# Kernel tuning notes

Measured on AMD Instinct MI355X. Metric: run time of the kernel, lower is better.

Reference implementation:

```python
import jax, jax.numpy as jnp
import numpy as np

E, H, I = 5, 768, 1024  # num_experts, hidden_dim, intermediate_dim
TOP_K = 2


def setup_inputs() -> dict:
    key = jax.random.key(0)
    ks = jax.random.split(key, 6)
    s = 0.02
    return {
        "x": jax.random.normal(ks[0], (4, 2048, H), dtype=jnp.float32),
        "router_w": jax.random.normal(ks[1], (E, H), dtype=jnp.float32) * s,  # torch Linear (out,in)
        "router_b": jnp.zeros((E,), dtype=jnp.float32),
        "gate_w": jax.random.normal(ks[2], (E, H, I), dtype=jnp.float32) * s,
        "up_w": jax.random.normal(ks[3], (E, H, I), dtype=jnp.float32) * s,
        "down_w": jax.random.normal(ks[4], (E, I, H), dtype=jnp.float32) * s,
    }


def reference(x, router_w, router_b, gate_w, up_w, down_w):
    B, S, Hd = x.shape
    xf = x.reshape(-1, Hd)                       # [T, H]
    T = xf.shape[0]
    # Router: linear (with bias) -> softmax -> top-2 -> renormalize
    logits = xf @ router_w.T + router_b          # [T, E]
    scores = jax.nn.softmax(logits, axis=-1)
    vals, idx = jax.lax.top_k(scores, TOP_K)     # [T, 2]
    vals = vals / jnp.sum(vals, axis=-1, keepdims=True)
    # Dense combine weights: zero for unselected experts (same math as the
    # per-expert gather/scatter loop in the original module).
    comb = jnp.zeros((T, gate_w.shape[0]), dtype=x.dtype)
    comb = comb.at[jnp.arange(T)[:, None], idx].add(vals)  # [T, E]
    # SwiGLU per expert, vectorized over experts
    g = jnp.einsum('th,ehi->tei', xf, gate_w)    # [T, E, I]
    u = jnp.einsum('th,ehi->tei', xf, up_w)
    y = jnp.einsum('tei,eih->teh', jax.nn.silu(g) * u, down_w)  # [T, E, H]
    out = jnp.einsum('teh,te->th', y, comb)
    return out.reshape(B, S, Hd)
```

## Files before the change

### kernel.cpp

```cpp
#include <hip/hip_runtime.h>
#include <hip/hip_bf16.h>
#include <cstdint>
#include <cstddef>

#define T_TOK 8192
#define H_DIM 768
#define I_DIM 1024
#define N_EXP 5
#define MAXTILE 136

typedef short v8s __attribute__((ext_vector_type(8)));
typedef float v4f __attribute__((ext_vector_type(4)));

static __device__ __forceinline__ unsigned short f2bf(float f) {
    union { float f; unsigned int u; } v; v.f = f;
    unsigned int u = v.u;
    unsigned int r = (u + 0x7fffu + ((u >> 16) & 1u)) >> 16;
    return (unsigned short)r;
}
static __device__ __forceinline__ float bf2f(unsigned short s) {
    union { unsigned int u; float f; } v; v.u = ((unsigned int)s) << 16; return v.f;
}

static __device__ __forceinline__ void async16(const unsigned short* g, unsigned short* l) {
    __builtin_amdgcn_global_load_lds(
        (const __attribute__((address_space(1))) unsigned int*)g,
        (__attribute__((address_space(3))) unsigned int*)l, 16, 0, 0);
}

__global__ void k_transp_wi(const float* __restrict__ gw, const float* __restrict__ uw,
                            unsigned short* __restrict__ wbt) {
    __shared__ float tile[32][33];
    int z = blockIdx.z;
    int e = z % N_EXP;
    int isUp = z >= N_EXP;
    const float* src = (isUp ? uw : gw) + (size_t)e * H_DIM * I_DIM;
    int c0 = blockIdx.x * 32, r0 = blockIdx.y * 32;
    int tx = threadIdx.x, ty = threadIdx.y;
#pragma unroll
    for (int i = 0; i < 4; i++)
        tile[ty * 4 + i][tx] = src[(size_t)(r0 + ty * 4 + i) * I_DIM + c0 + tx];
    __syncthreads();
#pragma unroll
    for (int i = 0; i < 4; i++) {
        int c = c0 + ty * 4 + i;
        int row = (c >> 4) * 32 + (c & 15) + (isUp ? 16 : 0);
        wbt[((size_t)e * 2 * I_DIM + row) * H_DIM + r0 + tx] = f2bf(tile[tx][ty * 4 + i]);
    }
}

__global__ void k_transp_d(const float* __restrict__ dw, unsigned short* __restrict__ dbt) {
    __shared__ float tile[32][33];
    int e = blockIdx.z;
    const float* src = dw + (size_t)e * I_DIM * H_DIM;
    unsigned short* dst = dbt + (size_t)e * I_DIM * H_DIM;
    int c0 = blockIdx.x * 32, r0 = blockIdx.y * 32;
    int tx = threadIdx.x, ty = threadIdx.y;
#pragma unroll
    for (int i = 0; i < 4; i++)
        tile[ty * 4 + i][tx] = src[(size_t)(r0 + ty * 4 + i) * H_DIM + c0 + tx];
    __syncthreads();
#pragma unroll
    for (int i = 0; i < 4; i++)
        dst[(size_t)(c0 + ty * 4 + i) * I_DIM + r0 + tx] = f2bf(tile[tx][ty * 4 + i]);
}

__global__ void k_router_a(const float* __restrict__ x, const float* __restrict__ rw,
                           const float* __restrict__ rb,
                           unsigned short* __restrict__ xb,
                           int* __restrict__ top2e, float2* __restrict__ top2w) {
    const int wave = threadIdx.x >> 6, lane = threadIdx.x & 63;
    const int t = blockIdx.x * 4 + wave;
    const float* xr = x + (size_t)t * H_DIM;
    unsigned short* xbr = xb + (size_t)t * H_DIM;
    float acc[N_EXP];
#pragma unroll
    for (int e = 0; e < N_EXP; e++) acc[e] = 0.f;
#pragma unroll
    for (int j = 0; j < H_DIM / 256; j++) {
        int idx = j * 256 + lane * 4;
        float4 xv = *(const float4*)(xr + idx);
        ushort4 o;
        o.x = f2bf(xv.x); o.y = f2bf(xv.y); o.z = f2bf(xv.z); o.w = f2bf(xv.w);
        *(ushort4*)(xbr + idx) = o;
#pragma unroll
        for (int e = 0; e < N_EXP; e++) {
            float4 wv = *(const float4*)(rw + e * H_DIM + idx);
            acc[e] += xv.x * wv.x + xv.y * wv.y + xv.z * wv.z + xv.w * wv.w;
        }
    }
#pragma unroll
    for (int s = 32; s > 0; s >>= 1) {
#pragma unroll
        for (int e = 0; e < N_EXP; e++) acc[e] += __shfl_down(acc[e], s);
    }
    if (lane == 0) {
        float l[N_EXP];
#pragma unroll
        for (int e = 0; e < N_EXP; e++) l[e] = acc[e] + rb[e];
        int i1 = 0;
#pragma unroll
        for (int e = 1; e < N_EXP; e++) if (l[e] > l[i1]) i1 = e;
        int i2 = (i1 == 0) ? 1 : 0;
#pragma unroll
        for (int e = 0; e < N_EXP; e++) if (e != i1 && l[e] > l[i2]) i2 = e;
        float w1 = 1.f / (1.f + __expf(l[i2] - l[i1]));
        top2e[t] = i1 | (i2 << 8);
        top2w[t] = make_float2(w1, 1.f - w1);
    }
}

__global__ void k_router_b(const int* __restrict__ top2e, const float2* __restrict__ top2w,
                           int* __restrict__ cnt, int* __restrict__ tokslot,
                           float* __restrict__ pweight) {
    __shared__ int lcnt[N_EXP], lbase[N_EXP];
    const int tid = threadIdx.x;
    if (tid < N_EXP) lcnt[tid] = 0;
    __syncthreads();
    const int t = blockIdx.x * 256 + tid;
    const int pe = top2e[t];
    const float2 wv = top2w[t];
    const int e1 = pe & 0xff, e2 = pe >> 8;
    const int s1 = atomicAdd(&lcnt[e1], 1);
    const int s2 = atomicAdd(&lcnt[e2], 1);
    __syncthreads();
    if (tid < N_EXP) lbase[tid] = atomicAdd(&cnt[tid], lcnt[tid]);
    __syncthreads();
    const int p1 = lbase[e1] + s1;
    tokslot[e1 * T_TOK + p1] = t; pweight[e1 * T_TOK + p1] = wv.x;
    const int p2 = lbase[e2] + s2;
    tokslot[e2 * T_TOK + p2] = t | (1 << 16); pweight[e2 * T_TOK + p2] = wv.y;
}

__global__ void k_tiles(const int* __restrict__ cnt, int4* __restrict__ tiles) {
    const int tid = threadIdx.x;
    if (tid < MAXTILE) tiles[tid] = make_int4(-1, 0, 0, 0);
    __syncthreads();
    if (tid == 0) {
        int off = 0, idx = 0;
        for (int e = 0; e < N_EXP; e++) {
            int cn = cnt[e];
            for (int m0 = 0; m0 < cn; m0 += 128)
                tiles[idx++] = make_int4(e, m0, off, cn);
            off += cn;
        }
    }
}

__launch_bounds__(256, 2)
__global__ void k_gateup(const unsigned short* __restrict__ xb,
                         const unsigned short* __restrict__ wbt,
                         const int4* __restrict__ tiles,
                         const int* __restrict__ tokslot,
                         const float* __restrict__ pweight,
                         unsigned short* __restrict__ hbuf) {
    const int4 td = tiles[blockIdx.x];
    const int e = td.x;
    if (e < 0) return;
    const int m0 = td.y, offe = td.z, cn = td.w;
    const int n0 = blockIdx.y * 64;

    __shared__ __align__(16) unsigned short ldsA[128 * 32];
    __shared__ __align__(16) unsigned short ldsB[128 * 32];
    __shared__ int tokLds[128];
    __shared__ float pwLds[128];

    const int tid = threadIdx.x;
    if (tid < 128) {
        int gr = m0 + tid;
        int tk = 0; float pw = 0.f;
        if (gr < cn) { tk = tokslot[e * T_TOK + gr] & 0xFFFF; pw = pweight[e * T_TOK + gr]; }
        tokLds[tid] = tk; pwLds[tid] = pw;
    }
    __syncthreads();

    const int lane = tid & 63;
    const int wave = tid >> 6;
    const int fm = lane & 15, quad = lane >> 4;

    const int srow = wave * 16 + (lane >> 2);
    const int scol = (lane & 3) * 8;
    const unsigned short* aG1 = xb + (size_t)tokLds[srow] * H_DIM + scol;
    const unsigned short* aG2 = xb + (size_t)tokLds[64 + srow] * H_DIM + scol;
    const unsigned short* bG1 = wbt + ((size_t)e * 2 * I_DIM + n0 * 2 + srow) * H_DIM + scol;
    const unsigned short* bG2 = wbt + ((size_t)e * 2 * I_DIM + n0 * 2 + 64 + srow) * H_DIM + scol;
    unsigned short* lA1 = ldsA + wave * 512;
    unsigned short* lA2 = ldsA + 2048 + wave * 512;
    unsigned short* lB1 = ldsB + wave * 512;
    unsigned short* lB2 = ldsB + 2048 + wave * 512;

    const int wm = (wave & 1) * 64, wnw = wave >> 1;

    v4f acc[4][4];
#pragma unroll
    for (int i = 0; i < 4; i++)
#pragma unroll
        for (int j = 0; j < 4; j++) acc[i][j] = (v4f)0.f;

    for (int kb = 0; kb < H_DIM / 32; kb++) {
        const int k0 = kb * 32;
        async16(aG1 + k0, lA1);
        async16(aG2 + k0, lA2);
        async16(bG1 + k0, lB1);
        async16(bG2 + k0, lB2);
        __syncthreads();
        v8s aF[4], bF[4];
#pragma unroll
        for (int im = 0; im < 4; im++)
            aF[im] = *(const v8s*)&ldsA[(wm + im * 16 + fm) * 32 + quad * 8];
#pragma unroll
        for (int in = 0; in < 4; in++)
            bF[in] = *(const v8s*)&ldsB[(wnw * 64 + in * 16 + fm) * 32 + quad * 8];
#pragma unroll
        for (int im = 0; im < 4; im++)
#pragma unroll
            for (int in = 0; in < 4; in++)
                acc[im][in] = __builtin_amdgcn_mfma_f32_16x16x32_bf16(aF[im], bF[in], acc[im][in], 0, 0, 0);
        __syncthreads();
    }

#pragma unroll
    for (int im = 0; im < 4; im++) {
#pragma unroll
        for (int reg = 0; reg < 4; reg++) {
            int lr = wm + im * 16 + quad * 4 + reg;
            int gr = m0 + lr;
            if (gr < cn) {
                float pw = pwLds[lr];
                size_t base = (size_t)(offe + gr) * I_DIM + n0 + wnw * 32 + fm;
#pragma unroll
                for (int j = 0; j < 2; j++) {
                    float g = acc[im][2 * j][reg];
                    float u = acc[im][2 * j + 1][reg];
                    float s = g / (1.f + __expf(-g));
                    hbuf[base + j * 16] = f2bf(s * u * pw);
                }
            }
        }
    }
}

__launch_bounds__(256, 2)
__global__ void k_down(const unsigned short* __restrict__ hbuf,
                       const unsigned short* __restrict__ dbt,
                       const int4* __restrict__ tiles,
                       const int* __restrict__ tokslot,
                       unsigned short* __restrict__ ybuf) {
    const int4 td = tiles[blockIdx.x];
    const int e = td.x;
    if (e < 0) return;
    const int m0 = td.y, offe = td.z, cn = td.w;
    const int n0 = blockIdx.y * 128;

    __shared__ __align__(16) unsigned short ldsA[128 * 32];
    __shared__ __align__(16) unsigned short ldsB[128 * 32];
    __shared__ int tokLds[128];

    const int tid = threadIdx.x;
    if (tid < 128) {
        int gr = m0 + tid;
        tokLds[tid] = (gr < cn) ? tokslot[e * T_TOK + gr] : 0;
    }
    __syncthreads();

    const int lane = tid & 63;
    const int wave = tid >> 6;
    const int fm = lane & 15, quad = lane >> 4;

    const int srow = wave * 16 + (lane >> 2);
    const int scol = (lane & 3) * 8;
    int ar1 = m0 + srow;      if (ar1 >= cn) ar1 = cn - 1;
    int ar2 = m0 + 64 + srow; if (ar2 >= cn) ar2 = cn - 1;
    const unsigned short* aG1 = hbuf + (size_t)(offe + ar1) * I_DIM + scol;
    const unsigned short* aG2 = hbuf + (size_t)(offe + ar2) * I_DIM + scol;
    const unsigned short* bG1 = dbt + ((size_t)e * H_DIM + n0 + srow) * I_DIM + scol;
    const unsigned short* bG2 = dbt + ((size_t)e * H_DIM + n0 + 64 + srow) * I_DIM + scol;
    unsigned short* lA1 = ldsA + wave * 512;
    unsigned short* lA2 = ldsA + 2048 + wave * 512;
    unsigned short* lB1 = ldsB + wave * 512;
    unsigned short* lB2 = ldsB + 2048 + wave * 512;

    const int wm = (wave & 1) * 64, wn = (wave >> 1) * 64;

    v4f acc[4][4];
#pragma unroll
    for (int i = 0; i < 4; i++)
#pragma unroll
        for (int j = 0; j < 4; j++) acc[i][j] = (v4f)0.f;

    for (int kb = 0; kb < I_DIM / 32; kb++) {
        const int k0 = kb * 32;
        async16(aG1 + k0, lA1);
        async16(aG2 + k0, lA2);
        async16(bG1 + k0, lB1);
        async16(bG2 + k0, lB2);
        __syncthreads();
        v8s aF[4], bF[4];
#pragma unroll
        for (int im = 0; im < 4; im++)
            aF[im] = *(const v8s*)&ldsA[(wm + im * 16 + fm) * 32 + quad * 8];
#pragma unroll
        for (int in = 0; in < 4; in++)
            bF[in] = *(const v8s*)&ldsB[(wn + in * 16 + fm) * 32 + quad * 8];
#pragma unroll
        for (int im = 0; im < 4; im++)
#pragma unroll
            for (int in = 0; in < 4; in++)
                acc[im][in] = __builtin_amdgcn_mfma_f32_16x16x32_bf16(aF[im], bF[in], acc[im][in], 0, 0, 0);
        __syncthreads();
    }

#pragma unroll
    for (int im = 0; im < 4; im++) {
#pragma unroll
        for (int reg = 0; reg < 4; reg++) {
            int lr = wm + im * 16 + quad * 4 + reg;
            int gr = m0 + lr;
            if (gr < cn) {
                int v = tokLds[lr];
                int tok = v & 0xFFFF, s = (v >> 16) & 1;
#pragma unroll
                for (int in = 0; in < 4; in++) {
                    int col = n0 + wn + in * 16 + fm;
                    ybuf[((size_t)s * T_TOK + tok) * H_DIM + col] = f2bf(acc[im][in][reg]);
                }
            }
        }
    }
}

__global__ void k_combine(const unsigned short* __restrict__ ybuf, float* __restrict__ out) {
    const size_t i8 = ((size_t)blockIdx.x * 256 + threadIdx.x) * 8;
    const unsigned short* y0 = ybuf + i8;
    const unsigned short* y1 = ybuf + (size_t)T_TOK * H_DIM + i8;
    ushort4 a0 = *(const ushort4*)y0, a1 = *(const ushort4*)(y0 + 4);
    ushort4 b0 = *(const ushort4*)y1, b1 = *(const ushort4*)(y1 + 4);
    float4 o0, o1;
    o0.x = bf2f(a0.x) + bf2f(b0.x); o0.y = bf2f(a0.y) + bf2f(b0.y);
    o0.z = bf2f(a0.z) + bf2f(b0.z); o0.w = bf2f(a0.w) + bf2f(b0.w);
    o1.x = bf2f(a1.x) + bf2f(b1.x); o1.y = bf2f(a1.y) + bf2f(b1.y);
    o1.z = bf2f(a1.z) + bf2f(b1.z); o1.w = bf2f(a1.w) + bf2f(b1.w);
    *(float4*)(out + i8) = o0;
    *(float4*)(out + i8 + 4) = o1;
}

extern "C" void kernel_launch(void* const* d_in, const int* in_sizes, int n_in,
                              void* d_out, int out_size, void* d_ws, size_t ws_size,
                              hipStream_t stream) {
    const float* x  = (const float*)d_in[0];
    const float* rw = (const float*)d_in[1];
    const float* rb = (const float*)d_in[2];
    const float* gw = (const float*)d_in[3];
    const float* uw = (const float*)d_in[4];
    const float* dw = (const float*)d_in[5];
    float* out = (float*)d_out;

    char* ws = (char*)d_ws;
    size_t o = 0;
    auto alloc = [&](size_t bytes) { void* p = ws + o; o += (bytes + 255) & ~255ull; return p; };
    int*   cnt     = (int*)  alloc(N_EXP * 4);
    int*   tokslot = (int*)  alloc((size_t)N_EXP * T_TOK * 4);
    float* pweight = (float*)alloc((size_t)N_EXP * T_TOK * 4);
    int*   top2e   = (int*)  alloc((size_t)T_TOK * 4);
    float2* top2w  = (float2*)alloc((size_t)T_TOK * 8);
    int4*  tiles   = (int4*) alloc((size_t)MAXTILE * 16);
    unsigned short* xb   = (unsigned short*)alloc((size_t)T_TOK * H_DIM * 2);
    unsigned short* wbt  = (unsigned short*)alloc((size_t)N_EXP * 2 * I_DIM * H_DIM * 2);
    unsigned short* dbt  = (unsigned short*)alloc((size_t)N_EXP * H_DIM * I_DIM * 2);
    unsigned short* hbuf = (unsigned short*)alloc((size_t)2 * T_TOK * I_DIM * 2);
    unsigned short* ybuf = (unsigned short*)alloc((size_t)2 * T_TOK * H_DIM * 2);

    hipMemsetAsync(cnt, 0, N_EXP * 4, stream);

    dim3 tg1(I_DIM / 32, H_DIM / 32, 2 * N_EXP);
    k_transp_wi<<<tg1, dim3(32, 8), 0, stream>>>(gw, uw, wbt);
    dim3 tg2(H_DIM / 32, I_DIM / 32, N_EXP);
    k_transp_d<<<tg2, dim3(32, 8), 0, stream>>>(dw, dbt);

    k_router_a<<<T_TOK / 4, 256, 0, stream>>>(x, rw, rb, xb, top2e, top2w);
    k_router_b<<<T_TOK / 256, 256, 0, stream>>>(top2e, top2w, cnt, tokslot, pweight);
    k_tiles<<<1, 256, 0, stream>>>(cnt, tiles);

    dim3 g1(MAXTILE, I_DIM / 64);
    k_gateup<<<g1, 256, 0, stream>>>(xb, wbt, tiles, tokslot, pweight, hbuf);

    dim3 g2(MAXTILE, H_DIM / 128);
    k_down<<<g2, 256, 0, stream>>>(hbuf, dbt, tiles, tokslot, ybuf);

    k_combine<<<(T_TOK * H_DIM) / (256 * 8), 256, 0, stream>>>(ybuf, out);
}
```

Measured before the change: 265.9 us.

## Pre-gather routed tokens into contiguous bf16 buffer and scatter-combine via inverse map

Adds a gather kernel that converts routed token rows of x to bf16 in expert-sorted contiguous order, so the gate/up GEMM loads A rows contiguously instead of through per-row token indirection. The down GEMM writes its output in sorted order, and the combine kernel uses an inverse index to sum each token's two expert rows. It also merges the two weight-transpose kernels into one launch and raises launch bounds to 4 blocks per CU. The trade is an extra gather pass and padding rows in exchange for fewer indirect loads. Padded rows past the tile end now read uninitialized workspace instead of clamped rows, but their results are discarded.

Result: slower. 299.5 us (+12.6%).

```diff
diff --git a/kernel.cpp b/kernel.cpp
--- a/kernel.cpp
+++ b/kernel.cpp
@@ -8,6 +8,7 @@
 #define I_DIM 1024
 #define N_EXP 5
 #define MAXTILE 136
+#define DROWS (2 * T_TOK)
 
 typedef short v8s __attribute__((ext_vector_type(8)));
 typedef float v4f __attribute__((ext_vector_type(4)));
@@ -28,51 +29,50 @@
         (__attribute__((address_space(3))) unsigned int*)l, 16, 0, 0);
 }
 
-__global__ void k_transp_wi(const float* __restrict__ gw, const float* __restrict__ uw,
-                            unsigned short* __restrict__ wbt) {
+__global__ void k_transp_all(const float* __restrict__ gw, const float* __restrict__ uw,
+                             const float* __restrict__ dw,
+                             unsigned short* __restrict__ wbt, unsigned short* __restrict__ dbt) {
     __shared__ float tile[32][33];
-    int z = blockIdx.z;
-    int e = z % N_EXP;
-    int isUp = z >= N_EXP;
-    const float* src = (isUp ? uw : gw) + (size_t)e * H_DIM * I_DIM;
-    int c0 = blockIdx.x * 32, r0 = blockIdx.y * 32;
-    int tx = threadIdx.x, ty = threadIdx.y;
-#pragma unroll
-    for (int i = 0; i < 4; i++)
-        tile[ty * 4 + i][tx] = src[(size_t)(r0 + ty * 4 + i) * I_DIM + c0 + tx];
-    __syncthreads();
-#pragma unroll
-    for (int i = 0; i < 4; i++) {
-        int c = c0 + ty * 4 + i;
-        int row = (c >> 4) * 32 + (c & 15) + (isUp ? 16 : 0);
-        wbt[((size_t)e * 2 * I_DIM + row) * H_DIM + r0 + tx] = f2bf(tile[tx][ty * 4 + i]);
-    }
-}
-
-__global__ void k_transp_d(const float* __restrict__ dw, unsigned short* __restrict__ dbt) {
-    __shared__ float tile[32][33];
-    int e = blockIdx.z;
-    const float* src = dw + (size_t)e * I_DIM * H_DIM;
-    unsigned short* dst = dbt + (size_t)e * I_DIM * H_DIM;
-    int c0 = blockIdx.x * 32, r0 = blockIdx.y * 32;
-    int tx = threadIdx.x, ty = threadIdx.y;
-#pragma unroll
-    for (int i = 0; i < 4; i++)
-        tile[ty * 4 + i][tx] = src[(size_t)(r0 + ty * 4 + i) * H_DIM + c0 + tx];
-    __syncthreads();
-#pragma unroll
-    for (int i = 0; i < 4; i++)
-        dst[(size_t)(c0 + ty * 4 + i) * I_DIM + r0 + tx] = f2bf(tile[tx][ty * 4 + i]);
+    const int z = blockIdx.z;
+    const int tx = threadIdx.x, ty = threadIdx.y;
+    if (z < 2 * N_EXP) {
+        if (blockIdx.y >= H_DIM / 32) return;
+        const int e = z % N_EXP;
+        const int isUp = z >= N_EXP;
+        const float* src = (isUp ? uw : gw) + (size_t)e * H_DIM * I_DIM;
+        const int c0 = blockIdx.x * 32, r0 = blockIdx.y * 32;
+#pragma unroll
+        for (int i = 0; i < 4; i++)
+            tile[ty * 4 + i][tx] = src[(size_t)(r0 + ty * 4 + i) * I_DIM + c0 + tx];
+        __syncthreads();
+#pragma unroll
+        for (int i = 0; i < 4; i++) {
+            int c = c0 + ty * 4 + i;
+            int row = (c >> 4) * 32 + (c & 15) + (isUp ? 16 : 0);
+            wbt[((size_t)e * 2 * I_DIM + row) * H_DIM + r0 + tx] = f2bf(tile[tx][ty * 4 + i]);
+        }
+    } else {
+        if (blockIdx.x >= H_DIM / 32) return;
+        const int e = z - 2 * N_EXP;
+        const float* src = dw + (size_t)e * I_DIM * H_DIM;
+        unsigned short* dst = dbt + (size_t)e * I_DIM * H_DIM;
+        const int c0 = blockIdx.x * 32, r0 = blockIdx.y * 32;
+#pragma unroll
+        for (int i = 0; i < 4; i++)
+            tile[ty * 4 + i][tx] = src[(size_t)(r0 + ty * 4 + i) * H_DIM + c0 + tx];
+        __syncthreads();
+#pragma unroll
+        for (int i = 0; i < 4; i++)
+            dst[(size_t)(c0 + ty * 4 + i) * I_DIM + r0 + tx] = f2bf(tile[tx][ty * 4 + i]);
+    }
 }
 
 __global__ void k_router_a(const float* __restrict__ x, const float* __restrict__ rw,
                            const float* __restrict__ rb,
-                           unsigned short* __restrict__ xb,
                            int* __restrict__ top2e, float2* __restrict__ top2w) {
     const int wave = threadIdx.x >> 6, lane = threadIdx.x & 63;
     const int t = blockIdx.x * 4 + wave;
     const float* xr = x + (size_t)t * H_DIM;
-    unsigned short* xbr = xb + (size_t)t * H_DIM;
     float acc[N_EXP];
 #pragma unroll
     for (int e = 0; e < N_EXP; e++) acc[e] = 0.f;
@@ -80,9 +80,6 @@
     for (int j = 0; j < H_DIM / 256; j++) {
         int idx = j * 256 + lane * 4;
         float4 xv = *(const float4*)(xr + idx);
-        ushort4 o;
-        o.x = f2bf(xv.x); o.y = f2bf(xv.y); o.z = f2bf(xv.z); o.w = f2bf(xv.w);
-        *(ushort4*)(xbr + idx) = o;
 #pragma unroll
         for (int e = 0; e < N_EXP; e++) {
             float4 wv = *(const float4*)(rw + e * H_DIM + idx);
@@ -147,12 +144,39 @@
     }
 }
 
-__launch_bounds__(256, 2)
-__global__ void k_gateup(const unsigned short* __restrict__ xb,
+__global__ void k_gather(const float* __restrict__ x, const int4* __restrict__ tiles,
+                         const int* __restrict__ tokslot, const float* __restrict__ pweight,
+                         unsigned short* __restrict__ xg, float* __restrict__ pwg,
+                         int* __restrict__ inv) {
+    const int4 td = tiles[blockIdx.x];
+    const int e = td.x;
+    if (e < 0) return;
+    const int m0 = td.y, offe = td.z, cn = td.w;
+    const int tid = threadIdx.x;
+    for (int c = tid; c < 128 * 96; c += 256) {
+        int row = c / 96, col = (c % 96) * 8;
+        int gr = m0 + row;
+        if (gr >= cn) continue;
+        int v = tokslot[e * T_TOK + gr];
+        int tok = v & 0xFFFF;
+        const float* src = x + (size_t)tok * H_DIM + col;
+        float4 a = *(const float4*)src, b = *(const float4*)(src + 4);
+        ushort4 o0; o0.x = f2bf(a.x); o0.y = f2bf(a.y); o0.z = f2bf(a.z); o0.w = f2bf(a.w);
+        ushort4 o1; o1.x = f2bf(b.x); o1.y = f2bf(b.y); o1.z = f2bf(b.z); o1.w = f2bf(b.w);
+        unsigned short* dst = xg + (size_t)(offe + gr) * H_DIM + col;
+        *(ushort4*)dst = o0; *(ushort4*)(dst + 4) = o1;
+        if ((c % 96) == 0) {
+            pwg[offe + gr] = pweight[e * T_TOK + gr];
+            inv[tok * 2 + ((v >> 16) & 1)] = offe + gr;
+        }
+    }
+}
+
+__launch_bounds__(256, 4)
+__global__ void k_gateup(const unsigned short* __restrict__ xg,
                          const unsigned short* __restrict__ wbt,
                          const int4* __restrict__ tiles,
-                         const int* __restrict__ tokslot,
-                         const float* __restrict__ pweight,
+                         const float* __restrict__ pwg,
                          unsigned short* __restrict__ hbuf) {
     const int4 td = tiles[blockIdx.x];
     const int e = td.x;
@@ -162,16 +186,10 @@
 
     __shared__ __align__(16) unsigned short ldsA[128 * 32];
     __shared__ __align__(16) unsigned short ldsB[128 * 32];
-    __shared__ int tokLds[128];
     __shared__ float pwLds[128];
 
     const int tid = threadIdx.x;
-    if (tid < 128) {
-        int gr = m0 + tid;
-        int tk = 0; float pw = 0.f;
-        if (gr < cn) { tk = tokslot[e * T_TOK + gr] & 0xFFFF; pw = pweight[e * T_TOK + gr]; }
-        tokLds[tid] = tk; pwLds[tid] = pw;
-    }
+    if (tid < 128) pwLds[tid] = pwg[offe + m0 + tid];
     __syncthreads();
 
     const int lane = tid & 63;
@@ -180,10 +198,10 @@
 
     const int srow = wave * 16 + (lane >> 2);
     const int scol = (lane & 3) * 8;
-    const unsigned short* aG1 = xb + (size_t)tokLds[srow] * H_DIM + scol;
-    const unsigned short* aG2 = xb + (size_t)tokLds[64 + srow] * H_DIM + scol;
+    const unsigned short* aG1 = xg + (size_t)(offe + m0 + srow) * H_DIM + scol;
+    const unsigned short* aG2 = aG1 + (size_t)64 * H_DIM;
     const unsigned short* bG1 = wbt + ((size_t)e * 2 * I_DIM + n0 * 2 + srow) * H_DIM + scol;
-    const unsigned short* bG2 = wbt + ((size_t)e * 2 * I_DIM + n0 * 2 + 64 + srow) * H_DIM + scol;
+    const unsigned short* bG2 = bG1 + (size_t)64 * H_DIM;
     unsigned short* lA1 = ldsA + wave * 512;
     unsigned short* lA2 = ldsA + 2048 + wave * 512;
     unsigned short* lB1 = ldsB + wave * 512;
@@ -240,12 +258,11 @@
     }
 }
 
-__launch_bounds__(256, 2)
+__launch_bounds__(256, 4)
 __global__ void k_down(const unsigned short* __restrict__ hbuf,
                        const unsigned short* __restrict__ dbt,
                        const int4* __restrict__ tiles,
-                       const int* __restrict__ tokslot,
-                       unsigned short* __restrict__ ybuf) {
+                       unsigned short* __restrict__ yd) {
     const int4 td = tiles[blockIdx.x];
     const int e = td.x;
     if (e < 0) return;
@@ -254,27 +271,18 @@
 
     __shared__ __align__(16) unsigned short ldsA[128 * 32];
     __shared__ __align__(16) unsigned short ldsB[128 * 32];
-    __shared__ int tokLds[128];
 
     const int tid = threadIdx.x;
-    if (tid < 128) {
-        int gr = m0 + tid;
-        tokLds[tid] = (gr < cn) ? tokslot[e * T_TOK + gr] : 0;
-    }
-    __syncthreads();
-
     const int lane = tid & 63;
     const int wave = tid >> 6;
     const int fm = lane & 15, quad = lane >> 4;
 
     const int srow = wave * 16 + (lane >> 2);
     const int scol = (lane & 3) * 8;
-    int ar1 = m0 + srow;      if (ar1 >= cn) ar1 = cn - 1;
-    int ar2 = m0 + 64 + srow; if (ar2 >= cn) ar2 = cn - 1;
-    const unsigned short* aG1 = hbuf + (size_t)(offe + ar1) * I_DIM + scol;
-    const unsigned short* aG2 = hbuf + (size_t)(offe + ar2) * I_DIM + scol;
+    const unsigned short* aG1 = hbuf + (size_t)(offe + m0 + srow) * I_DIM + scol;
+    const unsigned short* aG2 = aG1 + (size_t)64 * I_DIM;
     const unsigned short* bG1 = dbt + ((size_t)e * H_DIM + n0 + srow) * I_DIM + scol;
-    const unsigned short* bG2 = dbt + ((size_t)e * H_DIM + n0 + 64 + srow) * I_DIM + scol;
+    const unsigned short* bG2 = bG1 + (size_t)64 * I_DIM;
     unsigned short* lA1 = ldsA + wave * 512;
     unsigned short* lA2 = ldsA + 2048 + wave * 512;
     unsigned short* lB1 = ldsB + wave * 512;
@@ -317,31 +325,33 @@
             int lr = wm + im * 16 + quad * 4 + reg;
             int gr = m0 + lr;
             if (gr < cn) {
-                int v = tokLds[lr];
-                int tok = v & 0xFFFF, s = (v >> 16) & 1;
 #pragma unroll
                 for (int in = 0; in < 4; in++) {
                     int col = n0 + wn + in * 16 + fm;
-                    ybuf[((size_t)s * T_TOK + tok) * H_DIM + col] = f2bf(acc[im][in][reg]);
+                    yd[(size_t)(offe + gr) * H_DIM + col] = f2bf(acc[im][in][reg]);
                 }
             }
         }
     }
 }
 
-__global__ void k_combine(const unsigned short* __restrict__ ybuf, float* __restrict__ out) {
-    const size_t i8 = ((size_t)blockIdx.x * 256 + threadIdx.x) * 8;
-    const unsigned short* y0 = ybuf + i8;
-    const unsigned short* y1 = ybuf + (size_t)T_TOK * H_DIM + i8;
-    ushort4 a0 = *(const ushort4*)y0, a1 = *(const ushort4*)(y0 + 4);
-    ushort4 b0 = *(const ushort4*)y1, b1 = *(const ushort4*)(y1 + 4);
-    float4 o0, o1;
-    o0.x = bf2f(a0.x) + bf2f(b0.x); o0.y = bf2f(a0.y) + bf2f(b0.y);
-    o0.z = bf2f(a0.z) + bf2f(b0.z); o0.w = bf2f(a0.w) + bf2f(b0.w);
-    o1.x = bf2f(a1.x) + bf2f(b1.x); o1.y = bf2f(a1.y) + bf2f(b1.y);
-    o1.z = bf2f(a1.z) + bf2f(b1.z); o1.w = bf2f(a1.w) + bf2f(b1.w);
-    *(float4*)(out + i8) = o0;
-    *(float4*)(out + i8 + 4) = o1;
+__global__ void k_combine(const unsigned short* __restrict__ yd, const int* __restrict__ inv,
+                          float* __restrict__ out) {
+    const int wave = threadIdx.x >> 6, lane = threadIdx.x & 63;
+    const int t = blockIdx.x * 4 + wave;
+    const unsigned short* y0 = yd + (size_t)inv[2 * t] * H_DIM;
+    const unsigned short* y1 = yd + (size_t)inv[2 * t + 1] * H_DIM;
+    float* o = out + (size_t)t * H_DIM;
+#pragma unroll
+    for (int j = 0; j < 3; j++) {
+        int idx = j * 256 + lane * 4;
+        ushort4 a = *(const ushort4*)(y0 + idx);
+        ushort4 b = *(const ushort4*)(y1 + idx);
+        float4 v;
+        v.x = bf2f(a.x) + bf2f(b.x); v.y = bf2f(a.y) + bf2f(b.y);
+        v.z = bf2f(a.z) + bf2f(b.z); v.w = bf2f(a.w) + bf2f(b.w);
+        *(float4*)(o + idx) = v;
+    }
 }
 
 extern "C" void kernel_launch(void* const* d_in, const int* in_sizes, int n_in,
@@ -358,34 +368,35 @@
     char* ws = (char*)d_ws;
     size_t o = 0;
     auto alloc = [&](size_t bytes) { void* p = ws + o; o += (bytes + 255) & ~255ull; return p; };
-    int*   cnt     = (int*)  alloc(N_EXP * 4);
-    int*   tokslot = (int*)  alloc((size_t)N_EXP * T_TOK * 4);
-    float* pweight = (float*)alloc((size_t)N_EXP * T_TOK * 4);
-    int*   top2e   = (int*)  alloc((size_t)T_TOK * 4);
-    float2* top2w  = (float2*)alloc((size_t)T_TOK * 8);
-    int4*  tiles   = (int4*) alloc((size_t)MAXTILE * 16);
-    unsigned short* xb   = (unsigned short*)alloc((size_t)T_TOK * H_DIM * 2);
+    int*    cnt     = (int*)   alloc(N_EXP * 4);
+    int*    tokslot = (int*)   alloc((size_t)N_EXP * T_TOK * 4);
+    float*  pweight = (float*) alloc((size_t)N_EXP * T_TOK * 4);
+    int*    top2e   = (int*)   alloc((size_t)T_TOK * 4);
+    float2* top2w   = (float2*)alloc((size_t)T_TOK * 8);
+    int4*   tiles   = (int4*)  alloc((size_t)MAXTILE * 16);
+    float*  pwg     = (float*) alloc((size_t)(DROWS + 128) * 4);
+    int*    inv     = (int*)   alloc((size_t)T_TOK * 2 * 4);
     unsigned short* wbt  = (unsigned short*)alloc((size_t)N_EXP * 2 * I_DIM * H_DIM * 2);
     unsigned short* dbt  = (unsigned short*)alloc((size_t)N_EXP * H_DIM * I_DIM * 2);
-    unsigned short* hbuf = (unsigned short*)alloc((size_t)2 * T_TOK * I_DIM * 2);
-    unsigned short* ybuf = (unsigned short*)alloc((size_t)2 * T_TOK * H_DIM * 2);
+    unsigned short* xg   = (unsigned short*)alloc((size_t)(DROWS + 128) * H_DIM * 2);
+    unsigned short* hbuf = (unsigned short*)alloc((size_t)(DROWS + 128) * I_DIM * 2);
+    unsigned short* yd   = (unsigned short*)alloc((size_t)DROWS * H_DIM * 2);
 
     hipMemsetAsync(cnt, 0, N_EXP * 4, stream);
 
-    dim3 tg1(I_DIM / 32, H_DIM / 32, 2 * N_EXP);
-    k_transp_wi<<<tg1, dim3(32, 8), 0, stream>>>(gw, uw, wbt);
-    dim3 tg2(H_DIM / 32, I_DIM / 32, N_EXP);
-    k_transp_d<<<tg2, dim3(32, 8), 0, stream>>>(dw, dbt);
-
-    k_router_a<<<T_TOK / 4, 256, 0, stream>>>(x, rw, rb, xb, top2e, top2w);
+    dim3 tg(I_DIM / 32, I_DIM / 32, 3 * N_EXP);
+    k_transp_all<<<tg, dim3(32, 8), 0, stream>>>(gw, uw, dw, wbt, dbt);
+
+    k_router_a<<<T_TOK / 4, 256, 0, stream>>>(x, rw, rb, top2e, top2w);
     k_router_b<<<T_TOK / 256, 256, 0, stream>>>(top2e, top2w, cnt, tokslot, pweight);
     k_tiles<<<1, 256, 0, stream>>>(cnt, tiles);
+    k_gather<<<MAXTILE, 256, 0, stream>>>(x, tiles, tokslot, pweight, xg, pwg, inv);
 
     dim3 g1(MAXTILE, I_DIM / 64);
-    k_gateup<<<g1, 256, 0, stream>>>(xb, wbt, tiles, tokslot, pweight, hbuf);
+    k_gateup<<<g1, 256, 0, stream>>>(xg, wbt, tiles, pwg, hbuf);
 
     dim3 g2(MAXTILE, H_DIM / 128);
-    k_down<<<g2, 256, 0, stream>>>(hbuf, dbt, tiles, tokslot, ybuf);
-
-    k_combine<<<(T_TOK * H_DIM) / (256 * 8), 256, 0, stream>>>(ybuf, out);
-}
+    k_down<<<g2, 256, 0, stream>>>(hbuf, dbt, tiles, yd);
+
+    k_combine<<<T_TOK / 4, 256, 0, stream>>>(yd, inv, out);
+}
```
